# Performance work log

Hardware: AMD Instinct MI355X
Metric: run time of the kernel (lower is better)

The kernel has to match this reference:

```python
import jax, jax.numpy as jnp
import numpy as np

# Module hyperparameters (from init_kwargs)
KH, KW = 3, 3
STRIDE_H = STRIDE_W = 1
PAD_H = PAD_W = 1
DIL_H = DIL_W = 1
DEFORM_GROUPS = 1
IN_CH, OUT_CH = 64, 64


def setup_inputs() -> dict:
    key = jax.random.key(0)
    k1, k2, k3, k4 = jax.random.split(key, 4)
    B, C, H, W = 4, IN_CH, 128, 128
    K = KH * KW
    x = jax.random.normal(k1, (B, C, H, W), dtype=jnp.float32)
    offset = jax.random.normal(k2, (B, DEFORM_GROUPS * 2 * K, H, W), dtype=jnp.float32)
    mask = jax.random.uniform(k3, (B, DEFORM_GROUPS * K, H, W), dtype=jnp.float32)
    stdv = 1.0 / np.sqrt(C * KH * KW)
    weight = jax.random.uniform(k4, (OUT_CH, C, KH, KW), dtype=jnp.float32,
                                minval=-stdv, maxval=stdv)
    bias = jnp.zeros((OUT_CH,), dtype=jnp.float32)
    return {"x": x, "offset": offset, "mask": mask, "weight": weight, "bias": bias}


def _bilinear_gather(img, ys, xs):
    """img: [N,Cg,H,W]; ys,xs: [N,K,Ho,Wo] absolute pixel coords.
    Returns [N,K,Ho,Wo,Cg]; zero padding outside, matches torch grid_sample
    (align_corners=False, padding_mode='zeros')."""
    N, Cg, H, W = img.shape
    y0f = jnp.floor(ys)
    x0f = jnp.floor(xs)
    wy = (ys - y0f)[..., None]
    wx = (xs - x0f)[..., None]
    y0 = y0f.astype(jnp.int32)
    x0 = x0f.astype(jnp.int32)
    b = jnp.arange(N)[:, None, None, None]

    def g(yi, xi):
        valid = (yi >= 0) & (yi < H) & (xi >= 0) & (xi < W)
        v = img[b, :, jnp.clip(yi, 0, H - 1), jnp.clip(xi, 0, W - 1)]  # [N,K,Ho,Wo,Cg]
        return jnp.where(valid[..., None], v, jnp.zeros((), img.dtype))

    v00 = g(y0, x0)
    v01 = g(y0, x0 + 1)
    v10 = g(y0 + 1, x0)
    v11 = g(y0 + 1, x0 + 1)
    return (v00 * (1 - wy) * (1 - wx) + v01 * (1 - wy) * wx
            + v10 * wy * (1 - wx) + v11 * wy * wx)


def _mdcn(x, offset, mask, weight, bias):
    B, C, H, W = x.shape
    O = weight.shape[0]
    K = KH * KW
    G = DEFORM_GROUPS
    Cg = C // G
    Ho = (H + 2 * PAD_H - (DIL_H * (KH - 1) + 1)) // STRIDE_H + 1
    Wo = (W + 2 * PAD_W - (DIL_W * (KW - 1) + 1)) // STRIDE_W + 1

    base_y = jnp.arange(Ho, dtype=x.dtype) * STRIDE_H - PAD_H          # [Ho]
    base_x = jnp.arange(Wo, dtype=x.dtype) * STRIDE_W - PAD_W          # [Wo]
    ky = (jnp.arange(K) // KW).astype(x.dtype) * DIL_H                 # [K]
    kx = (jnp.arange(K) % KW).astype(x.dtype) * DIL_W                  # [K]

    off = offset.reshape(B, G, K, 2, Ho, Wo)
    sy = (base_y[None, None, None, :, None] + ky[None, None, :, None, None]
          + off[:, :, :, 0])                                           # [B,G,K,Ho,Wo]
    sx = (base_x[None, None, None, None, :] + kx[None, None, :, None, None]
          + off[:, :, :, 1])

    img = x.reshape(B * G, Cg, H, W)
    sampled = _bilinear_gather(img, sy.reshape(B * G, K, Ho, Wo),
                               sx.reshape(B * G, K, Ho, Wo))            # [B*G,K,Ho,Wo,Cg]
    sampled = sampled * mask.reshape(B * G, K, Ho, Wo)[..., None]
    sampled = sampled.reshape(B, G, K, Ho, Wo, Cg)

    w = weight.reshape(O, G, Cg, K)
    out = jnp.einsum('bgkhwc,ogck->bohw', sampled, w)
    return out + bias[None, :, None, None]


def reference(x, offset, mask, weight, bias):
    return _mdcn(x, offset, mask, weight, bias)
```

## Files before the change

### kernel.cpp

```cpp
#include <hip/hip_runtime.h>
#include <hip/hip_bf16.h>
#include <math.h>

constexpr int B = 4, C = 64, H = 128, W = 128, K = 9, O = 64;
constexpr int HXW = H * W;

typedef short short8 __attribute__((ext_vector_type(8)));
typedef float f32x4 __attribute__((ext_vector_type(4)));

static __device__ __forceinline__ short f2bf(float v) {
    __hip_bfloat16 h = __float2bfloat16(v);
    return (short)__builtin_bit_cast(unsigned short, h);
}
static __device__ __forceinline__ float bf2f(short s) {
    unsigned int u = ((unsigned int)(unsigned short)s) << 16;
    return __builtin_bit_cast(float, u);
}

__global__ void wt_kernel(const float* __restrict__ weight, float* __restrict__ wt) {
    int idx = blockIdx.x * 256 + threadIdx.x;
    if (idx >= K * C * O) return;
    int o = idx & 63;
    int c = (idx >> 6) & 63;
    int k = idx >> 12;
    wt[idx] = weight[(o * C + c) * K + k];
}

__global__ __launch_bounds__(256) void mdcn_nchw(
        const float* __restrict__ x, const float* __restrict__ offset,
        const float* __restrict__ mask, const float* __restrict__ wt,
        const float* __restrict__ bias, float* __restrict__ out) {
    int pid = blockIdx.x * 256 + threadIdx.x;
    int b = pid >> 14;
    int hw = pid & (HXW - 1);
    int h = hw >> 7;
    int w = hw & 127;
    float acc[O];
#pragma unroll
    for (int o = 0; o < O; ++o) acc[o] = bias[o];
#pragma unroll 1
    for (int k = 0; k < K; ++k) {
        float offy = offset[((size_t)(b * 2 * K + 2 * k)) * HXW + hw];
        float offx = offset[((size_t)(b * 2 * K + 2 * k + 1)) * HXW + hw];
        float m    = mask[((size_t)(b * K + k)) * HXW + hw];
        float sy = (float)(h - 1 + k / 3) + offy;
        float sx = (float)(w - 1 + k % 3) + offx;
        float y0f = floorf(sy), x0f = floorf(sx);
        float wy = sy - y0f, wx = sx - x0f;
        int y0 = (int)y0f, x0 = (int)x0f;
        int y1 = y0 + 1, x1 = x0 + 1;
        bool vy0 = (y0 >= 0) & (y0 < H), vy1 = (y1 >= 0) & (y1 < H);
        bool vx0 = (x0 >= 0) & (x0 < W), vx1 = (x1 >= 0) & (x1 < W);
        float w00 = (vy0 & vx0) ? (1.0f - wy) * (1.0f - wx) * m : 0.0f;
        float w01 = (vy0 & vx1) ? (1.0f - wy) * wx * m : 0.0f;
        float w10 = (vy1 & vx0) ? wy * (1.0f - wx) * m : 0.0f;
        float w11 = (vy1 & vx1) ? wy * wx * m : 0.0f;
        int y0c = min(max(y0, 0), H - 1), y1c = min(max(y1, 0), H - 1);
        int x0c = min(max(x0, 0), W - 1), x1c = min(max(x1, 0), W - 1);
        const float* p00 = x + (size_t)b * C * HXW + y0c * W + x0c;
        const float* p01 = x + (size_t)b * C * HXW + y0c * W + x1c;
        const float* p10 = x + (size_t)b * C * HXW + y1c * W + x0c;
        const float* p11 = x + (size_t)b * C * HXW + y1c * W + x1c;
        const float* wk = wt + k * C * O;
#pragma unroll 1
        for (int c0 = 0; c0 < C; c0 += 4) {
            float v[4];
#pragma unroll
            for (int j = 0; j < 4; ++j) {
                size_t cs = (size_t)(c0 + j) * HXW;
                v[j] = w00 * p00[cs] + w01 * p01[cs] + w10 * p10[cs] + w11 * p11[cs];
            }
            const float* wr = wk + c0 * O;
#pragma unroll
            for (int j = 0; j < 4; ++j)
#pragma unroll
                for (int o = 0; o < O; ++o) acc[o] = fmaf(wr[j * O + o], v[j], acc[o]);
        }
    }
#pragma unroll
    for (int o = 0; o < O; ++o) out[((size_t)(b * O + o)) * HXW + hw] = acc[o];
}

constexpr int XT_BLOCKS = B * HXW / 128;
__global__ __launch_bounds__(256) void prep_kernel(
        const float* __restrict__ x, const float* __restrict__ weight,
        short* __restrict__ xbt, short* __restrict__ wtb2) {
    int bid = blockIdx.x;
    if (bid < XT_BLOCKS) {
        __shared__ float lds[128 * 65];
        int t = threadIdx.x;
        int P = bid * 128;
        int b = P >> 14;
        int hw0 = P & (HXW - 1);
        int px = t & 127;
        int hf = t >> 7;
        const float* src = x + (size_t)b * C * HXW + hw0 + px;
#pragma unroll
        for (int cc = 0; cc < 32; ++cc) {
            int ch = hf * 32 + cc;
            lds[px * 65 + ch] = src[(size_t)ch * HXW];
        }
        __syncthreads();
        short* dst = xbt + ((size_t)b * HXW + hw0 + px) * 64 + hf * 32;
        const float* row = lds + px * 65 + hf * 32;
#pragma unroll
        for (int j = 0; j < 4; ++j) {
            short8 pk;
#pragma unroll
            for (int e = 0; e < 8; ++e) pk[e] = f2bf(row[j * 8 + e]);
            *(short8*)(dst + j * 8) = pk;
        }
    } else {
        int idx = (bid - XT_BLOCKS) * 256 + threadIdx.x;
        if (idx < K * O * C) {
            int e = idx & 7;
            int lane = (idx >> 3) & 63;
            int s = (idx >> 9) & 7;
            int k = idx >> 12;
            int ml = lane & 15, kg = lane >> 4;
            int nf = s & 3, ks = s >> 2;
            int o = nf * 16 + ml;
            int c = ks * 32 + kg * 8 + e;
            wtb2[idx] = f2bf(weight[(o * C + c) * K + k]);
        }
    }
}

__global__ __launch_bounds__(256, 2) void mdcn_bf16(
        const short* __restrict__ xbt,
        const float* __restrict__ offset,
        const float* __restrict__ mask,
        const short* __restrict__ wtb2,
        const float* __restrict__ bias,
        float* __restrict__ out) {
    __shared__ short Alds[4][32 * 64];

    int bid = blockIdx.x;
    int slab = bid & 7;
    int within = bid >> 3;
    int tid = threadIdx.x;
    int lane = tid & 63;
    int wid = tid >> 6;
    int ml = lane & 15, kg = lane >> 4;
    int p8 = lane >> 3, ch8 = lane & 7;
    int b = slab >> 1;
    int hwrow = (slab & 1) * 8192 + within * 128;
    int h = hwrow >> 7;
    int wvpx = wid * 32;
    short* Aw = &Alds[wid][0];

    f32x4 acc[2][4];
#pragma unroll
    for (int nf = 0; nf < 4; ++nf) {
        float bv = bias[nf * 16 + ml];
        acc[0][nf] = (f32x4){bv, bv, bv, bv};
        acc[1][nf] = (f32x4){bv, bv, bv, bv};
    }

    const short* xb = xbt + (size_t)b * HXW * 64;
    const float* offb = offset + (size_t)b * 2 * K * HXW;
    const float* mskb = mask + (size_t)b * K * HXW;

    float oy[4], ox[4], mm[4];
#pragma unroll
    for (int g = 0; g < 4; ++g) {
        int hw = hwrow + wvpx + g * 8 + p8;
        oy[g] = offb[hw];
        ox[g] = offb[(size_t)HXW + hw];
        mm[g] = mskb[hw];
    }

#pragma unroll 1
    for (int k = 0; k < K; ++k) {
        int ky = k / 3 - 1, kx = k % 3 - 1;

        float w00[4], w01[4], w10[4], w11[4];
        int r00[4], r01[4], r10[4], r11[4];
#pragma unroll
        for (int g = 0; g < 4; ++g) {
            int pl = g * 8 + p8;
            int w = wvpx + pl;
            float sy = (float)(h + ky) + oy[g];
            float sx = (float)(w + kx) + ox[g];
            float y0f = floorf(sy), x0f = floorf(sx);
            float wy = sy - y0f, wx = sx - x0f;
            int y0 = (int)y0f, x0 = (int)x0f;
            int y1 = y0 + 1, x1 = x0 + 1;
            bool vy0 = (y0 >= 0) & (y0 < H), vy1 = (y1 >= 0) & (y1 < H);
            bool vx0 = (x0 >= 0) & (x0 < W), vx1 = (x1 >= 0) & (x1 < W);
            float m = mm[g];
            w00[g] = (vy0 & vx0) ? (1.0f - wy) * (1.0f - wx) * m : 0.0f;
            w01[g] = (vy0 & vx1) ? (1.0f - wy) * wx * m : 0.0f;
            w10[g] = (vy1 & vx0) ? wy * (1.0f - wx) * m : 0.0f;
            w11[g] = (vy1 & vx1) ? wy * wx * m : 0.0f;
            int y0c = min(max(y0, 0), H - 1), y1c = min(max(y1, 0), H - 1);
            int x0c = min(max(x0, 0), W - 1), x1c = min(max(x1, 0), W - 1);
            r00[g] = y0c * W + x0c;
            r01[g] = y0c * W + x1c;
            r10[g] = y1c * W + x0c;
            r11[g] = y1c * W + x1c;
        }

        short8 c00[4], c01[4], c10[4], c11[4];
#pragma unroll
        for (int g = 0; g < 4; ++g) {
            c00[g] = *(const short8*)(xb + r00[g] * 64 + ch8 * 8);
            c01[g] = *(const short8*)(xb + r01[g] * 64 + ch8 * 8);
            c10[g] = *(const short8*)(xb + r10[g] * 64 + ch8 * 8);
            c11[g] = *(const short8*)(xb + r11[g] * 64 + ch8 * 8);
        }

        float oy2[4], ox2[4], mm2[4];
        if (k + 1 < K) {
#pragma unroll
            for (int g = 0; g < 4; ++g) {
                int hw = hwrow + wvpx + g * 8 + p8;
                oy2[g] = offb[(size_t)(2 * k + 2) * HXW + hw];
                ox2[g] = offb[(size_t)(2 * k + 3) * HXW + hw];
                mm2[g] = mskb[(size_t)(k + 1) * HXW + hw];
            }
        }
        __builtin_amdgcn_sched_barrier(0);

#pragma unroll
        for (int g = 0; g < 4; ++g) {
            int pl = g * 8 + p8;
            short8 pk;
#pragma unroll
            for (int e = 0; e < 8; ++e)
                pk[e] = f2bf(w00[g] * bf2f(c00[g][e]) + w01[g] * bf2f(c01[g][e]) +
                             w10[g] * bf2f(c10[g][e]) + w11[g] * bf2f(c11[g][e]));
            *(short8*)(Aw + pl * 64 + ((ch8 ^ (pl & 7)) * 8)) = pk;
        }

#pragma unroll
        for (int ks = 0; ks < 2; ++ks) {
            short8 bfr[4];
#pragma unroll
            for (int nf = 0; nf < 4; ++nf)
                bfr[nf] = *(const short8*)(wtb2 + ((size_t)((k * 8 + ks * 4 + nf) * 64 + lane)) * 8);
            short8 af[2];
#pragma unroll
            for (int mf = 0; mf < 2; ++mf) {
                int row = mf * 16 + ml;
                af[mf] = *(const short8*)(Aw + row * 64 + (((ks * 4 + kg) ^ (row & 7)) * 8));
            }
#pragma unroll
            for (int mf = 0; mf < 2; ++mf)
#pragma unroll
                for (int nf = 0; nf < 4; ++nf)
                    acc[mf][nf] = __builtin_amdgcn_mfma_f32_16x16x32_bf16(
                        af[mf], bfr[nf], acc[mf][nf], 0, 0, 0);
        }

        if (k + 1 < K) {
#pragma unroll
            for (int g = 0; g < 4; ++g) { oy[g] = oy2[g]; ox[g] = ox2[g]; mm[g] = mm2[g]; }
        }
    }

    int hwb = hwrow + wvpx;
#pragma unroll
    for (int mf = 0; mf < 2; ++mf)
#pragma unroll
        for (int nf = 0; nf < 4; ++nf) {
            size_t ob = ((size_t)(b * O + nf * 16 + ml)) * HXW + hwb + mf * 16 + kg * 4;
            *(float4*)(out + ob) = __builtin_bit_cast(float4, acc[mf][nf]);
        }
}

extern "C" void kernel_launch(void* const* d_in, const int* in_sizes, int n_in,
                              void* d_out, int out_size, void* d_ws, size_t ws_size,
                              hipStream_t stream) {
    const float* x      = (const float*)d_in[0];
    const float* offset = (const float*)d_in[1];
    const float* mask   = (const float*)d_in[2];
    const float* weight = (const float*)d_in[3];
    const float* bias   = (const float*)d_in[4];
    float* out = (float*)d_out;

    short* wtb2 = (short*)d_ws;
    short* xbt  = (short*)((char*)d_ws + 73728);
    size_t need = 73728 + (size_t)B * HXW * 64 * sizeof(short);

    if (ws_size >= need) {
        int wtb_blocks = (K * O * C + 255) / 256;
        prep_kernel<<<XT_BLOCKS + wtb_blocks, 256, 0, stream>>>(x, weight, xbt, wtb2);
        mdcn_bf16<<<512, 256, 0, stream>>>(xbt, offset, mask, wtb2, bias, out);
    } else {
        float* wt = (float*)d_ws;
        wt_kernel<<<(K * C * O + 255) / 256, 256, 0, stream>>>(weight, wt);
        mdcn_nchw<<<(B * HXW) / 256, 256, 0, stream>>>(x, offset, mask, wt, bias, out);
    }
}
```

Baseline: 41.86 us.

## Switch to fp16 packed interpolation and halve per-wave pixel tile

Converts the staged input and weights from bf16 to fp16, so bilinear interpolation can run as packed half-precision vector math instead of per-element bf16 to fp32 conversions, and uses the f16 MFMA. It also halves each wave's pixel tile from 32 to 16, doubling the grid to 1024 blocks and raising the occupancy hint to 4 blocks per CU to increase parallelism and latency hiding. In exchange, interpolation is accumulated in fp16, which costs precision, and each weight fragment load feeds fewer MFMAs.

```diff
diff --git a/kernel.cpp b/kernel.cpp
--- a/kernel.cpp
+++ b/kernel.cpp
@@ -5,17 +5,8 @@
 constexpr int B = 4, C = 64, H = 128, W = 128, K = 9, O = 64;
 constexpr int HXW = H * W;
 
-typedef short short8 __attribute__((ext_vector_type(8)));
+typedef _Float16 half8 __attribute__((ext_vector_type(8)));
 typedef float f32x4 __attribute__((ext_vector_type(4)));
-
-static __device__ __forceinline__ short f2bf(float v) {
-    __hip_bfloat16 h = __float2bfloat16(v);
-    return (short)__builtin_bit_cast(unsigned short, h);
-}
-static __device__ __forceinline__ float bf2f(short s) {
-    unsigned int u = ((unsigned int)(unsigned short)s) << 16;
-    return __builtin_bit_cast(float, u);
-}
 
 __global__ void wt_kernel(const float* __restrict__ weight, float* __restrict__ wt) {
     int idx = blockIdx.x * 256 + threadIdx.x;
@@ -84,7 +75,7 @@
 constexpr int XT_BLOCKS = B * HXW / 128;
 __global__ __launch_bounds__(256) void prep_kernel(
         const float* __restrict__ x, const float* __restrict__ weight,
-        short* __restrict__ xbt, short* __restrict__ wtb2) {
+        _Float16* __restrict__ xht, _Float16* __restrict__ wth) {
     int bid = blockIdx.x;
     if (bid < XT_BLOCKS) {
         __shared__ float lds[128 * 65];
@@ -101,14 +92,14 @@
             lds[px * 65 + ch] = src[(size_t)ch * HXW];
         }
         __syncthreads();
-        short* dst = xbt + ((size_t)b * HXW + hw0 + px) * 64 + hf * 32;
+        _Float16* dst = xht + ((size_t)b * HXW + hw0 + px) * 64 + hf * 32;
         const float* row = lds + px * 65 + hf * 32;
 #pragma unroll
         for (int j = 0; j < 4; ++j) {
-            short8 pk;
-#pragma unroll
-            for (int e = 0; e < 8; ++e) pk[e] = f2bf(row[j * 8 + e]);
-            *(short8*)(dst + j * 8) = pk;
+            half8 pk;
+#pragma unroll
+            for (int e = 0; e < 8; ++e) pk[e] = (_Float16)row[j * 8 + e];
+            *(half8*)(dst + j * 8) = pk;
         }
     } else {
         int idx = (bid - XT_BLOCKS) * 256 + threadIdx.x;
@@ -121,19 +112,19 @@
             int nf = s & 3, ks = s >> 2;
             int o = nf * 16 + ml;
             int c = ks * 32 + kg * 8 + e;
-            wtb2[idx] = f2bf(weight[(o * C + c) * K + k]);
-        }
-    }
-}
-
-__global__ __launch_bounds__(256, 2) void mdcn_bf16(
-        const short* __restrict__ xbt,
+            wth[idx] = (_Float16)weight[(o * C + c) * K + k];
+        }
+    }
+}
+
+__global__ __launch_bounds__(256, 4) void mdcn_f16(
+        const _Float16* __restrict__ xht,
         const float* __restrict__ offset,
         const float* __restrict__ mask,
-        const short* __restrict__ wtb2,
+        const _Float16* __restrict__ wth,
         const float* __restrict__ bias,
         float* __restrict__ out) {
-    __shared__ short Alds[4][32 * 64];
+    __shared__ _Float16 Alds[4][16 * 64];
 
     int bid = blockIdx.x;
     int slab = bid & 7;
@@ -144,27 +135,27 @@
     int ml = lane & 15, kg = lane >> 4;
     int p8 = lane >> 3, ch8 = lane & 7;
     int b = slab >> 1;
-    int hwrow = (slab & 1) * 8192 + within * 128;
-    int h = hwrow >> 7;
-    int wvpx = wid * 32;
-    short* Aw = &Alds[wid][0];
-
-    f32x4 acc[2][4];
+    int hwbase = (slab & 1) * 8192 + within * 64;
+    int h = hwbase >> 7;
+    int wvpx = wid * 16;
+    int wbase = (hwbase & 127) + wvpx;
+    _Float16* Aw = &Alds[wid][0];
+
+    f32x4 acc[4];
 #pragma unroll
     for (int nf = 0; nf < 4; ++nf) {
         float bv = bias[nf * 16 + ml];
-        acc[0][nf] = (f32x4){bv, bv, bv, bv};
-        acc[1][nf] = (f32x4){bv, bv, bv, bv};
-    }
-
-    const short* xb = xbt + (size_t)b * HXW * 64;
+        acc[nf] = (f32x4){bv, bv, bv, bv};
+    }
+
+    const _Float16* xb = xht + (size_t)b * HXW * 64;
     const float* offb = offset + (size_t)b * 2 * K * HXW;
     const float* mskb = mask + (size_t)b * K * HXW;
 
-    float oy[4], ox[4], mm[4];
-#pragma unroll
-    for (int g = 0; g < 4; ++g) {
-        int hw = hwrow + wvpx + g * 8 + p8;
+    float oy[2], ox[2], mm[2];
+#pragma unroll
+    for (int g = 0; g < 2; ++g) {
+        int hw = hwbase + wvpx + g * 8 + p8;
         oy[g] = offb[hw];
         ox[g] = offb[(size_t)HXW + hw];
         mm[g] = mskb[hw];
@@ -174,12 +165,12 @@
     for (int k = 0; k < K; ++k) {
         int ky = k / 3 - 1, kx = k % 3 - 1;
 
-        float w00[4], w01[4], w10[4], w11[4];
-        int r00[4], r01[4], r10[4], r11[4];
-#pragma unroll
-        for (int g = 0; g < 4; ++g) {
+        float w00[2], w01[2], w10[2], w11[2];
+        int r00[2], r01[2], r10[2], r11[2];
+#pragma unroll
+        for (int g = 0; g < 2; ++g) {
             int pl = g * 8 + p8;
-            int w = wvpx + pl;
+            int w = wbase + pl;
             float sy = (float)(h + ky) + oy[g];
             float sx = (float)(w + kx) + ox[g];
             float y0f = floorf(sy), x0f = floorf(sx);
@@ -201,20 +192,20 @@
             r11[g] = y1c * W + x1c;
         }
 
-        short8 c00[4], c01[4], c10[4], c11[4];
-#pragma unroll
-        for (int g = 0; g < 4; ++g) {
-            c00[g] = *(const short8*)(xb + r00[g] * 64 + ch8 * 8);
-            c01[g] = *(const short8*)(xb + r01[g] * 64 + ch8 * 8);
-            c10[g] = *(const short8*)(xb + r10[g] * 64 + ch8 * 8);
-            c11[g] = *(const short8*)(xb + r11[g] * 64 + ch8 * 8);
-        }
-
-        float oy2[4], ox2[4], mm2[4];
+        half8 c00[2], c01[2], c10[2], c11[2];
+#pragma unroll
+        for (int g = 0; g < 2; ++g) {
+            c00[g] = *(const half8*)(xb + r00[g] * 64 + ch8 * 8);
+            c01[g] = *(const half8*)(xb + r01[g] * 64 + ch8 * 8);
+            c10[g] = *(const half8*)(xb + r10[g] * 64 + ch8 * 8);
+            c11[g] = *(const half8*)(xb + r11[g] * 64 + ch8 * 8);
+        }
+
+        float oy2[2], ox2[2], mm2[2];
         if (k + 1 < K) {
 #pragma unroll
-            for (int g = 0; g < 4; ++g) {
-                int hw = hwrow + wvpx + g * 8 + p8;
+            for (int g = 0; g < 2; ++g) {
+                int hw = hwbase + wvpx + g * 8 + p8;
                 oy2[g] = offb[(size_t)(2 * k + 2) * HXW + hw];
                 ox2[g] = offb[(size_t)(2 * k + 3) * HXW + hw];
                 mm2[g] = mskb[(size_t)(k + 1) * HXW + hw];
@@ -223,50 +214,38 @@
         __builtin_amdgcn_sched_barrier(0);
 
 #pragma unroll
-        for (int g = 0; g < 4; ++g) {
+        for (int g = 0; g < 2; ++g) {
             int pl = g * 8 + p8;
-            short8 pk;
-#pragma unroll
-            for (int e = 0; e < 8; ++e)
-                pk[e] = f2bf(w00[g] * bf2f(c00[g][e]) + w01[g] * bf2f(c01[g][e]) +
-                             w10[g] * bf2f(c10[g][e]) + w11[g] * bf2f(c11[g][e]));
-            *(short8*)(Aw + pl * 64 + ((ch8 ^ (pl & 7)) * 8)) = pk;
+            _Float16 h00 = (_Float16)w00[g], h01 = (_Float16)w01[g];
+            _Float16 h10 = (_Float16)w10[g], h11 = (_Float16)w11[g];
+            half8 pk = c00[g] * h00 + c01[g] * h01 + c10[g] * h10 + c11[g] * h11;
+            *(half8*)(Aw + pl * 64 + ((ch8 ^ (pl & 7)) * 8)) = pk;
         }
 
 #pragma unroll
         for (int ks = 0; ks < 2; ++ks) {
-            short8 bfr[4];
+            half8 bfr[4];
 #pragma unroll
             for (int nf = 0; nf < 4; ++nf)
-                bfr[nf] = *(const short8*)(wtb2 + ((size_t)((k * 8 + ks * 4 + nf) * 64 + lane)) * 8);
-            short8 af[2];
-#pragma unroll
-            for (int mf = 0; mf < 2; ++mf) {
-                int row = mf * 16 + ml;
-                af[mf] = *(const short8*)(Aw + row * 64 + (((ks * 4 + kg) ^ (row & 7)) * 8));
-            }
-#pragma unroll
-            for (int mf = 0; mf < 2; ++mf)
-#pragma unroll
-                for (int nf = 0; nf < 4; ++nf)
-                    acc[mf][nf] = __builtin_amdgcn_mfma_f32_16x16x32_bf16(
-                        af[mf], bfr[nf], acc[mf][nf], 0, 0, 0);
+                bfr[nf] = *(const half8*)(wth + ((size_t)((k * 8 + ks * 4 + nf) * 64 + lane)) * 8);
+            half8 af = *(const half8*)(Aw + ml * 64 + (((ks * 4 + kg) ^ (ml & 7)) * 8));
+#pragma unroll
+            for (int nf = 0; nf < 4; ++nf)
+                acc[nf] = __builtin_amdgcn_mfma_f32_16x16x32_f16(af, bfr[nf], acc[nf], 0, 0, 0);
         }
 
         if (k + 1 < K) {
 #pragma unroll
-            for (int g = 0; g < 4; ++g) { oy[g] = oy2[g]; ox[g] = ox2[g]; mm[g] = mm2[g]; }
-        }
-    }
-
-    int hwb = hwrow + wvpx;
-#pragma unroll
-    for (int mf = 0; mf < 2; ++mf)
-#pragma unroll
-        for (int nf = 0; nf < 4; ++nf) {
-            size_t ob = ((size_t)(b * O + nf * 16 + ml)) * HXW + hwb + mf * 16 + kg * 4;
-            *(float4*)(out + ob) = __builtin_bit_cast(float4, acc[mf][nf]);
-        }
+            for (int g = 0; g < 2; ++g) { oy[g] = oy2[g]; ox[g] = ox2[g]; mm[g] = mm2[g]; }
+        }
+    }
+
+    int hwb = hwbase + wvpx + kg * 4;
+#pragma unroll
+    for (int nf = 0; nf < 4; ++nf) {
+        size_t ob = ((size_t)(b * O + nf * 16 + ml)) * HXW + hwb;
+        *(float4*)(out + ob) = __builtin_bit_cast(float4, acc[nf]);
+    }
 }
 
 extern "C" void kernel_launch(void* const* d_in, const int* in_sizes, int n_in,
@@ -279,14 +258,14 @@
     const float* bias   = (const float*)d_in[4];
     float* out = (float*)d_out;
 
-    short* wtb2 = (short*)d_ws;
-    short* xbt  = (short*)((char*)d_ws + 73728);
-    size_t need = 73728 + (size_t)B * HXW * 64 * sizeof(short);
+    _Float16* wth = (_Float16*)d_ws;
+    _Float16* xht = (_Float16*)((char*)d_ws + 73728);
+    size_t need = 73728 + (size_t)B * HXW * 64 * sizeof(_Float16);
 
     if (ws_size >= need) {
-        int wtb_blocks = (K * O * C + 255) / 256;
-        prep_kernel<<<XT_BLOCKS + wtb_blocks, 256, 0, stream>>>(x, weight, xbt, wtb2);
-        mdcn_bf16<<<512, 256, 0, stream>>>(xbt, offset, mask, wtb2, bias, out);
+        int wth_blocks = (K * O * C + 255) / 256;
+        prep_kernel<<<XT_BLOCKS + wth_blocks, 256, 0, stream>>>(x, weight, xht, wth);
+        mdcn_f16<<<1024, 256, 0, stream>>>(xht, offset, mask, wth, bias, out);
     } else {
         float* wt = (float*)d_ws;
         wt_kernel<<<(K * C * O + 255) / 256, 256, 0, stream>>>(weight, wt);
```

Result: faster. 39.42 us (-5.8%).
